# Performance work log

Hardware: AMD Instinct MI355X
Metric: run time of the kernel (lower is better)

## Reference

```python
import jax, jax.numpy as jnp
import numpy as np

L, D, F, H = 6, 512, 2048, 8
DH = D // H
SCALE = DH ** -0.5
B, S = 2, 2048


def _ln(x, w, b):
    m = jnp.mean(x, axis=-1, keepdims=True)
    v = jnp.var(x, axis=-1, keepdims=True)
    return (x - m) * jax.lax.rsqrt(v + 1e-5) * w + b


def setup_inputs() -> dict:
    key = jax.random.key(0)
    ks = jax.random.split(key, 10)
    s = 0.02
    return {
        "x": jax.random.normal(ks[0], (B, S, D), jnp.float32),
        "mask": jnp.zeros((B, 1, 1, S), jnp.float32),
        "ln1_w": jnp.ones((L, D), jnp.float32),
        "ln1_b": jnp.zeros((L, D), jnp.float32),
        "in_w": s * jax.random.normal(ks[1], (L, D, 3 * D), jnp.float32),
        "in_b": jnp.zeros((L, 3 * D), jnp.float32),
        "out_w": s * jax.random.normal(ks[2], (L, D, D), jnp.float32),
        "out_b": jnp.zeros((L, D), jnp.float32),
        "ln2_w": jnp.ones((L, D), jnp.float32),
        "ln2_b": jnp.zeros((L, D), jnp.float32),
        "ffn1_w": s * jax.random.normal(ks[3], (L, D, F), jnp.float32),
        "ffn1_b": jnp.zeros((L, F), jnp.float32),
        "ffn2_w": s * jax.random.normal(ks[4], (L, F, D), jnp.float32),
        "ffn2_b": jnp.zeros((L, D), jnp.float32),
        "norm_w": jnp.ones((D,), jnp.float32),
        "norm_b": jnp.zeros((D,), jnp.float32),
    }


def reference(x, mask, ln1_w, ln1_b, in_w, in_b, out_w, out_b,
              ln2_w, ln2_b, ffn1_w, ffn1_b, ffn2_w, ffn2_b, norm_w, norm_b):
    def step(h, p):
        (l1w, l1b, iw, ib, ow, ob, l2w, l2b, f1w, f1b, f2w, f2b) = p
        # --- self-attention (pre-norm) ---
        y = _ln(h, l1w, l1b)
        proj = y @ iw + ib                       # [B,S,3D]
        q, k, v = jnp.split(proj, 3, axis=-1)    # each [B,S,D]
        q = q.reshape(B, S, H, DH)
        k = k.reshape(B, S, H, DH)
        v = v.reshape(B, S, H, DH)
        dot = jnp.einsum('bqhd,bkhd->bhqk', q * SCALE, k) + mask  # [B,H,S,S]
        att = jax.nn.softmax(dot, axis=-1)
        o = jnp.einsum('bhqk,bkhd->bqhd', att, v).reshape(B, S, D)
        h = o @ ow + ob + h
        # --- FFN (pre-norm) ---
        y = _ln(h, l2w, l2b)
        y = jax.nn.relu(y @ f1w + f1b) @ f2w + f2b
        return h + y, None

    params = (ln1_w, ln1_b, in_w, in_b, out_w, out_b,
              ln2_w, ln2_b, ffn1_w, ffn1_b, ffn2_w, ffn2_b)
    x, _ = jax.lax.scan(step, x, params)
    return _ln(x, norm_w, norm_b)
```

## Files before the change

kernel.cpp:

```cpp
#include <hip/hip_runtime.h>
#include <hip/hip_bf16.h>
#include <stdint.h>


typedef __bf16 bf16x8 __attribute__((ext_vector_type(8)));
typedef __bf16 bf16x4 __attribute__((ext_vector_type(4)));
typedef float f32x4 __attribute__((ext_vector_type(4)));
typedef unsigned short u16;
typedef unsigned short u16x8 __attribute__((ext_vector_type(8)));

#define NB 2
#define NS 2048
#define ND 512
#define NH 8
#define NDH 64
#define NF 2048
#define NL 6
#define NCHUNK 8
#define CK (NS / NCHUNK)
#define LOG2E 1.4426950408889634f
#define QSCALE (0.125f * LOG2E)

#if defined(__has_builtin)
#if __has_builtin(__builtin_amdgcn_global_load_lds)
#define HAVE_GLDS 1
#endif
#endif
#ifndef HAVE_GLDS
#define HAVE_GLDS 0
#endif

#if HAVE_GLDS
__device__ __forceinline__ void glds16(const u16* g, u16* l) {
  __builtin_amdgcn_global_load_lds(
      (const __attribute__((address_space(1))) unsigned int*)g,
      (__attribute__((address_space(3))) unsigned int*)l, 16, 0, 0);
}
#endif

__device__ __forceinline__ u16 f2bf(float f) {
  unsigned u = __float_as_uint(f);
  u += 0x7FFFu + ((u >> 16) & 1u);
  return (u16)(u >> 16);
}

__global__ __launch_bounds__(256) void wcvt_t(const float* __restrict__ src,
                                              u16* __restrict__ dst,
                                              int K, int N) {
  __shared__ float tile[32][33];
  int l = blockIdx.z;
  const float* s = src + (size_t)l * K * N;
  u16* d = dst + (size_t)l * K * N;
  int k0 = blockIdx.y * 32, n0 = blockIdx.x * 32;
  int tx = threadIdx.x, ty = threadIdx.y;
  for (int i = 0; i < 32; i += 8)
    tile[ty + i][tx] = s[(size_t)(k0 + ty + i) * N + n0 + tx];
  __syncthreads();
  for (int i = 0; i < 32; i += 8)
    d[(size_t)(n0 + ty + i) * K + k0 + tx] = f2bf(tile[tx][ty + i]);
}

template <int OUT_BF16>
__global__ __launch_bounds__(256) void ln_k(const float* __restrict__ x,
                                            const float* __restrict__ w,
                                            const float* __restrict__ b,
                                            void* __restrict__ out) {
  int row = blockIdx.x;
  int t = threadIdx.x;
  const float* xr = x + (size_t)row * ND;
  float2 v = ((const float2*)xr)[t];
  float s = v.x + v.y, ss = v.x * v.x + v.y * v.y;
  for (int o = 32; o > 0; o >>= 1) {
    s += __shfl_down(s, o);
    ss += __shfl_down(ss, o);
  }
  __shared__ float rs[4], rss[4];
  if ((t & 63) == 0) { rs[t >> 6] = s; rss[t >> 6] = ss; }
  __syncthreads();
  float S = rs[0] + rs[1] + rs[2] + rs[3];
  float SS = rss[0] + rss[1] + rss[2] + rss[3];
  float mean = S * (1.0f / ND);
  float var = SS * (1.0f / ND) - mean * mean;
  float rstd = rsqrtf(var + 1e-5f);
  float2 wv = ((const float2*)w)[t];
  float2 bv = ((const float2*)b)[t];
  float y0 = (v.x - mean) * rstd * wv.x + bv.x;
  float y1 = (v.y - mean) * rstd * wv.y + bv.y;
  if (OUT_BF16) {
    ushort2 p; p.x = f2bf(y0); p.y = f2bf(y1);
    ((ushort2*)out)[(size_t)row * (ND / 2) + t] = p;
  } else {
    float2 p; p.x = y0; p.y = y1;
    ((float2*)out)[(size_t)row * (ND / 2) + t] = p;
  }
}

template <int EPI, int BM, int BN, int BK, int KSPLIT = 1>
__global__ __launch_bounds__(256) void gemm_bt(const u16* __restrict__ A,
                                               const u16* __restrict__ Bt,
                                               const float* __restrict__ bias,
                                               const float* __restrict__ resid,
                                               void* __restrict__ C,
                                               int M, int N, int K) {
  constexpr int MT = BM / 32;
  constexpr int NT = BN / 32;
  constexpr int CB = BK / 8;
  constexpr int RPP = 2048 / BK;
  constexpr int AP = BM / RPP;
  constexpr int BP = BN / RPP;
  constexpr int KK = BK / 32;
  __shared__ u16 la[BM * BK];
  __shared__ u16 lb[BN * BK];
  int bm = blockIdx.y, bn = blockIdx.x;
  int kc = (KSPLIT > 1) ? blockIdx.z : 0;
  int klen = K / KSPLIT;
  int kbase = kc * klen;
  int t = threadIdx.x;
  int wave = t >> 6, lane = t & 63, quad = lane >> 4, l15 = lane & 15;
  int wm = (wave >> 1) * (BM / 2), wn = (wave & 1) * (BN / 2);
  f32x4 acc[MT][NT] = {};
  int srow = t / CB;
  int scol = ((t % CB) ^ (srow & (CB - 1))) * 8;
  const u16* Ag = A + (size_t)(bm * BM) * K + kbase;
  const u16* Bg = Bt + (size_t)(bn * BN) * K + kbase;
#if HAVE_GLDS
  u16* laB = la + wave * 512;
  u16* lbB = lb + wave * 512;
#endif
  for (int k0 = 0; k0 < klen; k0 += BK) {
    __syncthreads();
#if HAVE_GLDS
#pragma unroll
    for (int g = 0; g < AP; g++)
      glds16(&Ag[(size_t)(srow + g * RPP) * K + k0 + scol], laB + g * 2048);
#pragma unroll
    for (int g = 0; g < BP; g++)
      glds16(&Bg[(size_t)(srow + g * RPP) * K + k0 + scol], lbB + g * 2048);
#else
#pragma unroll
    for (int g = 0; g < AP; g++)
      *(bf16x8*)&la[(srow + g * RPP) * BK + (t % CB) * 8] =
          *(const bf16x8*)&Ag[(size_t)(srow + g * RPP) * K + k0 + scol];
#pragma unroll
    for (int g = 0; g < BP; g++)
      *(bf16x8*)&lb[(srow + g * RPP) * BK + (t % CB) * 8] =
          *(const bf16x8*)&Bg[(size_t)(srow + g * RPP) * K + k0 + scol];
#endif
    __syncthreads();
#pragma unroll
    for (int kk = 0; kk < KK; kk++) {
      bf16x8 af[MT], bfr[NT];
#pragma unroll
      for (int i = 0; i < MT; i++) {
        int row = wm + i * 16 + l15;
        af[i] = *(const bf16x8*)&la[row * BK + ((kk * 4 + quad) ^ (row & (CB - 1))) * 8];
      }
#pragma unroll
      for (int i = 0; i < NT; i++) {
        int row = wn + i * 16 + l15;
        bfr[i] = *(const bf16x8*)&lb[row * BK + ((kk * 4 + quad) ^ (row & (CB - 1))) * 8];
      }
#pragma unroll
      for (int mt = 0; mt < MT; mt++)
#pragma unroll
        for (int nt = 0; nt < NT; nt++)
          acc[mt][nt] = __builtin_amdgcn_mfma_f32_16x16x32_bf16(
              af[mt], bfr[nt], acc[mt][nt], 0, 0, 0);
    }
  }
#pragma unroll
  for (int mt = 0; mt < MT; mt++)
#pragma unroll
    for (int nt = 0; nt < NT; nt++) {
      int col = bn * BN + wn + nt * 16 + l15;
      float bcol = (EPI == 3 || EPI == 4) ? 0.f : bias[col];
#pragma unroll
      for (int r = 0; r < 4; r++) {
        int row = bm * BM + wm + mt * 16 + quad * 4 + r;
        float v = acc[mt][nt][r] + ((EPI == 3) ? bias[row] : bcol);
        if (EPI == 1) v = fmaxf(v, 0.f);
        if (EPI == 2)
          ((float*)C)[(size_t)row * N + col] = v + resid[(size_t)row * N + col];
        else if (EPI == 4)
          ((u16*)C)[(size_t)kc * M * N + (size_t)row * N + col] = f2bf(v);
        else
          ((u16*)C)[(size_t)row * N + col] = f2bf(v);
      }
    }
}

__global__ __launch_bounds__(256) void ksplit_red(const u16* __restrict__ part,
                                                  const float* __restrict__ bias,
                                                  const float* __restrict__ resid,
                                                  float* __restrict__ out) {
  int gt = blockIdx.x * 256 + threadIdx.x;
  int col = (gt & 63) * 8;
  int row = gt >> 6;
  size_t base = (size_t)row * ND + col;
  float acc[8];
#pragma unroll
  for (int j = 0; j < 8; j++) acc[j] = bias[col + j] + resid[base + j];
#pragma unroll
  for (int c = 0; c < 4; c++) {
    bf16x8 v = *(const bf16x8*)&part[(size_t)c * (NB * NS) * ND + base];
#pragma unroll
    for (int j = 0; j < 8; j++) acc[j] += (float)v[j];
  }
#pragma unroll
  for (int j = 0; j < 2; j++)
    *(float4*)&out[base + j * 4] =
        make_float4(acc[j * 4], acc[j * 4 + 1], acc[j * 4 + 2], acc[j * 4 + 3]);
}

__global__ __launch_bounds__(256) void attn_k(const u16* __restrict__ qk,
                                              const u16* __restrict__ vt,
                                              const float* __restrict__ mask,
                                              u16* __restrict__ opart,
                                              float* __restrict__ lbuf) {
  __shared__ u16 kt_s[64 * 64];
  __shared__ u16 vt_s[64 * 64];
  __shared__ u16 p_s[4][16 * 68];
  int bh = blockIdx.y;
  int b = bh >> 3, h = bh & 7;
  int qt = blockIdx.x;
  int c = blockIdx.z;
  int t = threadIdx.x;
  int wave = t >> 6, lane = t & 63, quad = lane >> 4, l15 = lane & 15;

  int qrow = qt * 64 + wave * 16 + l15;
  const u16* qbase = qk + ((size_t)(b * NS + qrow)) * (2 * ND) + h * NDH;
  bf16x8 qf[2];
  qf[0] = *(const bf16x8*)&qbase[quad * 8];
  qf[1] = *(const bf16x8*)&qbase[32 + quad * 8];
#pragma unroll
  for (int e = 0; e < 8; e++) {
    qf[0][e] = (__bf16)((float)qf[0][e] * QSCALE);
    qf[1][e] = (__bf16)((float)qf[1][e] * QSCALE);
  }
  bf16x8 ones;
#pragma unroll
  for (int e = 0; e < 8; e++) ones[e] = (__bf16)1.0f;

  f32x4 oacc[4] = {};
  f32x4 ls = {};

  int srow8 = t >> 3;
  int segsw = ((t & 7) ^ ((t >> 3) & 7)) * 8;
  const u16* kg0 = qk + ((size_t)(b * NS + srow8)) * (2 * ND) + ND + h * NDH + segsw;
  const u16* vg0 = vt + ((size_t)(h * NDH + srow8)) * (NB * NS) + b * NS + segsw;
#if HAVE_GLDS
  u16* ktB = kt_s + wave * 512;
  u16* vtB = vt_s + wave * 512;
#endif
  for (int kt0 = c * CK; kt0 < (c + 1) * CK; kt0 += 64) {
    float m2[4];
#pragma unroll
    for (int nt = 0; nt < 4; nt++)
      m2[nt] = mask[b * NS + kt0 + nt * 16 + l15] * LOG2E;
    __syncthreads();
#if HAVE_GLDS
    glds16(&kg0[(size_t)kt0 * (2 * ND)], ktB);
    glds16(&kg0[(size_t)(kt0 + 32) * (2 * ND)], ktB + 2048);
    glds16(&vg0[kt0], vtB);
    glds16(&vg0[kt0 + (size_t)32 * (NB * NS)], vtB + 2048);
#else
    *(bf16x8*)&kt_s[srow8 * 64 + (t & 7) * 8] =
        *(const bf16x8*)&kg0[(size_t)kt0 * (2 * ND)];
    *(bf16x8*)&kt_s[(srow8 + 32) * 64 + (t & 7) * 8] =
        *(const bf16x8*)&kg0[(size_t)(kt0 + 32) * (2 * ND)];
    *(bf16x8*)&vt_s[srow8 * 64 + (t & 7) * 8] = *(const bf16x8*)&vg0[kt0];
    *(bf16x8*)&vt_s[(srow8 + 32) * 64 + (t & 7) * 8] =
        *(const bf16x8*)&vg0[kt0 + (size_t)32 * (NB * NS)];
#endif
    __syncthreads();
    f32x4 sc[4] = {};
#pragma unroll
    for (int nt = 0; nt < 4; nt++) {
      int row = nt * 16 + l15;
      bf16x8 kf0 = *(const bf16x8*)&kt_s[row * 64 + (quad ^ (row & 7)) * 8];
      bf16x8 kf1 = *(const bf16x8*)&kt_s[row * 64 + ((quad + 4) ^ (row & 7)) * 8];
      sc[nt] = __builtin_amdgcn_mfma_f32_16x16x32_bf16(qf[0], kf0, sc[nt], 0, 0, 0);
      sc[nt] = __builtin_amdgcn_mfma_f32_16x16x32_bf16(qf[1], kf1, sc[nt], 0, 0, 0);
    }
    u16* pw = &p_s[wave][0];
#pragma unroll
    for (int nt = 0; nt < 4; nt++) {
#pragma unroll
      for (int rp = 0; rp < 2; rp++) {
        float2 pp;
        pp.x = __builtin_amdgcn_exp2f(sc[nt][2 * rp] + m2[nt]);
        pp.y = __builtin_amdgcn_exp2f(sc[nt][2 * rp + 1] + m2[nt]);
        __hip_bfloat162 bb = __float22bfloat162_rn(pp);
        ushort2 us = *reinterpret_cast<ushort2*>(&bb);
        pw[(quad * 4 + 2 * rp) * 68 + nt * 16 + l15] = us.x;
        pw[(quad * 4 + 2 * rp + 1) * 68 + nt * 16 + l15] = us.y;
      }
    }
    asm volatile("s_waitcnt lgkmcnt(0)" ::: "memory");
#pragma unroll
    for (int kk = 0; kk < 2; kk++) {
      bf16x4 plo = *(const bf16x4*)&pw[l15 * 68 + kk * 32 + quad * 8];
      bf16x4 phi = *(const bf16x4*)&pw[l15 * 68 + kk * 32 + quad * 8 + 4];
      bf16x8 pf = __builtin_shufflevector(plo, phi, 0, 1, 2, 3, 4, 5, 6, 7);
#pragma unroll
      for (int nt = 0; nt < 4; nt++) {
        int row = nt * 16 + l15;
        bf16x8 vf = *(const bf16x8*)&vt_s[row * 64 + ((kk * 4 + quad) ^ (row & 7)) * 8];
        oacc[nt] = __builtin_amdgcn_mfma_f32_16x16x32_bf16(pf, vf, oacc[nt], 0, 0, 0);
      }
      ls = __builtin_amdgcn_mfma_f32_16x16x32_bf16(pf, ones, ls, 0, 0, 0);
    }
  }
  u16* ob = opart + (((size_t)(c * NB * NH + bh) * NS) + qt * 64 + wave * 16) * NDH;
#pragma unroll
  for (int nt = 0; nt < 4; nt++)
#pragma unroll
    for (int r = 0; r < 4; r++)
      ob[(size_t)(quad * 4 + r) * NDH + nt * 16 + l15] = f2bf(oacc[nt][r]);
  if (l15 == 0) {
    size_t li = (size_t)(c * NB * NH + bh) * NS + qt * 64 + wave * 16 + quad * 4;
#pragma unroll
    for (int r = 0; r < 4; r++) lbuf[li + r] = ls[r];
  }
}

__global__ __launch_bounds__(256) void attn_merge(const u16* __restrict__ opart,
                                                  const float* __restrict__ lbuf,
                                                  u16* __restrict__ o) {
  int gt = blockIdx.x * 256 + threadIdx.x;
  int grp = gt & 7;
  int s = (gt >> 3) & (NS - 1);
  int bh = gt >> 14;
  float L = 0.f;
#pragma unroll
  for (int c = 0; c < NCHUNK; c++)
    L += lbuf[(size_t)(c * NB * NH + bh) * NS + s];
  float inv = 1.0f / L;
  float acc[8] = {};
#pragma unroll
  for (int c = 0; c < NCHUNK; c++) {
    bf16x8 ov = *(const bf16x8*)&opart[((size_t)(c * NB * NH + bh) * NS + s) * NDH + grp * 8];
#pragma unroll
    for (int j = 0; j < 8; j++) acc[j] += (float)ov[j];
  }
  u16x8 res;
#pragma unroll
  for (int j = 0; j < 8; j++) res[j] = f2bf(acc[j] * inv);
  int b = bh >> 3, h = bh & 7;
  *(u16x8*)&o[((size_t)(b * NS + s)) * ND + h * NDH + grp * 8] = res;
}

extern "C" void kernel_launch(void* const* d_in, const int* in_sizes, int n_in,
                              void* d_out, int out_size, void* d_ws, size_t ws_size,
                              hipStream_t stream) {
  const float* x = (const float*)d_in[0];
  const float* mask = (const float*)d_in[1];
  const float* ln1w = (const float*)d_in[2];
  const float* ln1b = (const float*)d_in[3];
  const float* in_w = (const float*)d_in[4];
  const float* in_b = (const float*)d_in[5];
  const float* out_w = (const float*)d_in[6];
  const float* out_b = (const float*)d_in[7];
  const float* ln2w = (const float*)d_in[8];
  const float* ln2b = (const float*)d_in[9];
  const float* f1w = (const float*)d_in[10];
  const float* f1b = (const float*)d_in[11];
  const float* f2w = (const float*)d_in[12];
  const float* f2b = (const float*)d_in[13];
  const float* normw = (const float*)d_in[14];
  const float* normb = (const float*)d_in[15];

  char* ws = (char*)d_ws;
  auto carve = [&](size_t bytes) {
    char* p = ws;
    ws += (bytes + 255) & ~(size_t)255;
    return p;
  };
  u16* wq_t = (u16*)carve((size_t)NL * 3 * ND * ND * 2);
  u16* wo_t = (u16*)carve((size_t)NL * ND * ND * 2);
  u16* w1_t = (u16*)carve((size_t)NL * NF * ND * 2);
  u16* w2_t = (u16*)carve((size_t)NL * ND * NF * 2);
  u16* ybuf = (u16*)carve((size_t)NB * NS * ND * 2);
  u16* qk = (u16*)carve((size_t)NB * NS * 2 * ND * 2);
  u16* vtb = (u16*)carve((size_t)ND * NB * NS * 2);
  u16* obuf = (u16*)carve((size_t)NB * NS * ND * 2);
  u16* ubuf = (u16*)carve((size_t)NB * NS * NF * 2);
  float* hA = (float*)carve((size_t)NB * NS * ND * 4);
  float* hB = (float*)carve((size_t)NB * NS * ND * 4);
  float* lbuf = (float*)carve((size_t)NCHUNK * NB * NH * NS * 4);
  u16* opart = (u16*)carve((size_t)NCHUNK * NB * NH * NS * NDH * 2);
  u16* pbuf = (u16*)carve((size_t)4 * NB * NS * ND * 2);

  const int M = NB * NS;
  dim3 tb(32, 8);
  wcvt_t<<<dim3(3 * ND / 32, ND / 32, NL), tb, 0, stream>>>(in_w, wq_t, ND, 3 * ND);
  wcvt_t<<<dim3(ND / 32, ND / 32, NL), tb, 0, stream>>>(out_w, wo_t, ND, ND);
  wcvt_t<<<dim3(NF / 32, ND / 32, NL), tb, 0, stream>>>(f1w, w1_t, ND, NF);
  wcvt_t<<<dim3(ND / 32, NF / 32, NL), tb, 0, stream>>>(f2w, w2_t, NF, ND);

  const float* hin = x;
  for (int l = 0; l < NL; l++) {
    ln_k<1><<<M, 256, 0, stream>>>(hin, ln1w + l * ND, ln1b + l * ND, ybuf);
    gemm_bt<0, 64, 128, 128><<<dim3(2 * ND / 128, M / 64), 256, 0, stream>>>(
        ybuf, wq_t + (size_t)l * 3 * ND * ND, in_b + l * 3 * ND, nullptr, qk,
        M, 2 * ND, ND);
    gemm_bt<3, 64, 64, 128><<<dim3(M / 64, ND / 64), 256, 0, stream>>>(
        wq_t + (size_t)l * 3 * ND * ND + (size_t)2 * ND * ND, ybuf,
        in_b + l * 3 * ND + 2 * ND, nullptr, vtb, ND, M, ND);
    attn_k<<<dim3(NS / 64, NB * NH, NCHUNK), 256, 0, stream>>>(
        qk, vtb, mask, opart, lbuf);
    attn_merge<<<(NB * NH * NS * 8) / 256, 256, 0, stream>>>(opart, lbuf, obuf);
    gemm_bt<2, 64, 64, 128><<<dim3(ND / 64, M / 64), 256, 0, stream>>>(
        obuf, wo_t + (size_t)l * ND * ND, out_b + l * ND, hin, hB, M, ND, ND);
    ln_k<1><<<M, 256, 0, stream>>>(hB, ln2w + l * ND, ln2b + l * ND, ybuf);
    gemm_bt<1, 128, 128, 64><<<dim3(NF / 128, M / 128), 256, 0, stream>>>(
        ybuf, w1_t + (size_t)l * NF * ND, f1b + l * NF, nullptr, ubuf, M, NF, ND);
    gemm_bt<4, 128, 128, 64, 4><<<dim3(ND / 128, M / 128, 4), 256, 0, stream>>>(
        ubuf, w2_t + (size_t)l * ND * NF, nullptr, nullptr, pbuf, M, ND, NF);
    ksplit_red<<<(M * ND / 8) / 256, 256, 0, stream>>>(
        pbuf, f2b + l * ND, hB, hA);
    hin = hA;
  }
  ln_k<0><<<M, 256, 0, stream>>>(hA, normw, normb, (float*)d_out);
}
```

Baseline: 849.3 us.

## Fuse QKV GEMMs, fold layernorms into split-K reductions, halve attention chunks

Merges the QK and V projection GEMMs into one launch that dispatches on block id. The out-projection becomes a 4-way split-K GEMM whose reduction kernel also adds bias and residual and applies the following layernorm. The FFN2 reduction likewise applies the next layer's LN1, or the final norm on the last layer. Attention key chunks drop from 8 to 4. The goal is fewer launches and fewer full-activation round trips, at the cost of bf16 partial-sum rounding in the out-projection and less parallelism in attention.

```diff
diff --git a/kernel.cpp b/kernel.cpp
--- a/kernel.cpp
+++ b/kernel.cpp
@@ -16,7 +16,7 @@
 #define NDH 64
 #define NF 2048
 #define NL 6
-#define NCHUNK 8
+#define NCHUNK 4
 #define CK (NS / NCHUNK)
 #define LOG2E 1.4426950408889634f
 #define QSCALE (0.125f * LOG2E)
@@ -60,11 +60,10 @@
     d[(size_t)(n0 + ty + i) * K + k0 + tx] = f2bf(tile[tx][ty + i]);
 }
 
-template <int OUT_BF16>
 __global__ __launch_bounds__(256) void ln_k(const float* __restrict__ x,
                                             const float* __restrict__ w,
                                             const float* __restrict__ b,
-                                            void* __restrict__ out) {
+                                            u16* __restrict__ out) {
   int row = blockIdx.x;
   int t = threadIdx.x;
   const float* xr = x + (size_t)row * ND;
@@ -84,24 +83,21 @@
   float rstd = rsqrtf(var + 1e-5f);
   float2 wv = ((const float2*)w)[t];
   float2 bv = ((const float2*)b)[t];
-  float y0 = (v.x - mean) * rstd * wv.x + bv.x;
-  float y1 = (v.y - mean) * rstd * wv.y + bv.y;
-  if (OUT_BF16) {
-    ushort2 p; p.x = f2bf(y0); p.y = f2bf(y1);
-    ((ushort2*)out)[(size_t)row * (ND / 2) + t] = p;
-  } else {
-    float2 p; p.x = y0; p.y = y1;
-    ((float2*)out)[(size_t)row * (ND / 2) + t] = p;
-  }
-}
-
-template <int EPI, int BM, int BN, int BK, int KSPLIT = 1>
-__global__ __launch_bounds__(256) void gemm_bt(const u16* __restrict__ A,
-                                               const u16* __restrict__ Bt,
-                                               const float* __restrict__ bias,
-                                               const float* __restrict__ resid,
-                                               void* __restrict__ C,
-                                               int M, int N, int K) {
+  ushort2 p;
+  p.x = f2bf((v.x - mean) * rstd * wv.x + bv.x);
+  p.y = f2bf((v.y - mean) * rstd * wv.y + bv.y);
+  ((ushort2*)out)[(size_t)row * (ND / 2) + t] = p;
+}
+
+template <int EPI, int BM, int BN, int BK, int KSPLIT>
+__device__ __forceinline__ void gemm_dev(u16* la, u16* lb,
+                                         const u16* __restrict__ A,
+                                         const u16* __restrict__ Bt,
+                                         const float* __restrict__ bias,
+                                         const float* __restrict__ resid,
+                                         void* __restrict__ C,
+                                         int M, int N, int K,
+                                         int bm, int bn, int kc, int t) {
   constexpr int MT = BM / 32;
   constexpr int NT = BN / 32;
   constexpr int CB = BK / 8;
@@ -109,13 +105,8 @@
   constexpr int AP = BM / RPP;
   constexpr int BP = BN / RPP;
   constexpr int KK = BK / 32;
-  __shared__ u16 la[BM * BK];
-  __shared__ u16 lb[BN * BK];
-  int bm = blockIdx.y, bn = blockIdx.x;
-  int kc = (KSPLIT > 1) ? blockIdx.z : 0;
   int klen = K / KSPLIT;
   int kbase = kc * klen;
-  int t = threadIdx.x;
   int wave = t >> 6, lane = t & 63, quad = lane >> 4, l15 = lane & 15;
   int wm = (wave >> 1) * (BM / 2), wn = (wave & 1) * (BN / 2);
   f32x4 acc[MT][NT] = {};
@@ -189,13 +180,51 @@
     }
 }
 
-__global__ __launch_bounds__(256) void ksplit_red(const u16* __restrict__ part,
-                                                  const float* __restrict__ bias,
-                                                  const float* __restrict__ resid,
-                                                  float* __restrict__ out) {
-  int gt = blockIdx.x * 256 + threadIdx.x;
-  int col = (gt & 63) * 8;
-  int row = gt >> 6;
+template <int EPI, int BM, int BN, int BK, int KSPLIT = 1>
+__global__ __launch_bounds__(256) void gemm_bt(const u16* __restrict__ A,
+                                               const u16* __restrict__ Bt,
+                                               const float* __restrict__ bias,
+                                               const float* __restrict__ resid,
+                                               void* __restrict__ C,
+                                               int M, int N, int K) {
+  __shared__ u16 la[BM * BK];
+  __shared__ u16 lb[BN * BK];
+  gemm_dev<EPI, BM, BN, BK, KSPLIT>(la, lb, A, Bt, bias, resid, C, M, N, K,
+                                    blockIdx.y, blockIdx.x,
+                                    (KSPLIT > 1) ? blockIdx.z : 0, threadIdx.x);
+}
+
+__global__ __launch_bounds__(256) void qkv_fused(const u16* __restrict__ y,
+                                                 const u16* __restrict__ wqk,
+                                                 const u16* __restrict__ wv,
+                                                 const float* __restrict__ inb,
+                                                 u16* __restrict__ qkout,
+                                                 u16* __restrict__ vtout) {
+  __shared__ u16 smem[(64 + 128) * 128];
+  int id = blockIdx.x, t = threadIdx.x;
+  const int M = NB * NS;
+  if (id < 512) {
+    gemm_dev<0, 64, 128, 128, 1>(smem, smem + 64 * 128, y, wqk, inb, nullptr,
+                                 qkout, M, 2 * ND, ND, id >> 3, id & 7, 0, t);
+  } else {
+    id -= 512;
+    gemm_dev<3, 64, 64, 128, 1>(smem, smem + 64 * 128, wv, y, inb + 2 * ND,
+                                nullptr, vtout, ND, M, ND, id >> 6, id & 63, 0, t);
+  }
+}
+
+template <int OUT_BF16>
+__global__ __launch_bounds__(256) void red_ln(const u16* __restrict__ part,
+                                              const float* __restrict__ bias,
+                                              const float* __restrict__ resid,
+                                              const float* __restrict__ lw,
+                                              const float* __restrict__ lbb,
+                                              float* __restrict__ hout,
+                                              void* __restrict__ yout) {
+  int t = threadIdx.x;
+  int row = blockIdx.x * 4 + (t >> 6);
+  int lane = t & 63;
+  int col = lane * 8;
   size_t base = (size_t)row * ND + col;
   float acc[8];
 #pragma unroll
@@ -206,10 +235,34 @@
 #pragma unroll
     for (int j = 0; j < 8; j++) acc[j] += (float)v[j];
   }
-#pragma unroll
-  for (int j = 0; j < 2; j++)
-    *(float4*)&out[base + j * 4] =
-        make_float4(acc[j * 4], acc[j * 4 + 1], acc[j * 4 + 2], acc[j * 4 + 3]);
+  *(float4*)&hout[base] = make_float4(acc[0], acc[1], acc[2], acc[3]);
+  *(float4*)&hout[base + 4] = make_float4(acc[4], acc[5], acc[6], acc[7]);
+  float s = 0.f, ss = 0.f;
+#pragma unroll
+  for (int j = 0; j < 8; j++) { s += acc[j]; ss += acc[j] * acc[j]; }
+  for (int o = 1; o < 64; o <<= 1) {
+    s += __shfl_xor(s, o);
+    ss += __shfl_xor(ss, o);
+  }
+  float mean = s * (1.0f / ND);
+  float var = ss * (1.0f / ND) - mean * mean;
+  float rstd = rsqrtf(var + 1e-5f);
+  float4 w0 = *(const float4*)&lw[col], w1 = *(const float4*)&lw[col + 4];
+  float4 b0 = *(const float4*)&lbb[col], b1 = *(const float4*)&lbb[col + 4];
+  float wv[8] = {w0.x, w0.y, w0.z, w0.w, w1.x, w1.y, w1.z, w1.w};
+  float bv[8] = {b0.x, b0.y, b0.z, b0.w, b1.x, b1.y, b1.z, b1.w};
+  float yv[8];
+#pragma unroll
+  for (int j = 0; j < 8; j++) yv[j] = (acc[j] - mean) * rstd * wv[j] + bv[j];
+  if (OUT_BF16) {
+    u16x8 res;
+#pragma unroll
+    for (int j = 0; j < 8; j++) res[j] = f2bf(yv[j]);
+    *(u16x8*)&((u16*)yout)[base] = res;
+  } else {
+    *(float4*)&((float*)yout)[base] = make_float4(yv[0], yv[1], yv[2], yv[3]);
+    *(float4*)&((float*)yout)[base + 4] = make_float4(yv[4], yv[5], yv[6], yv[7]);
+  }
 }
 
 __global__ __launch_bounds__(256) void attn_k(const u16* __restrict__ qk,
@@ -398,28 +451,32 @@
   wcvt_t<<<dim3(NF / 32, ND / 32, NL), tb, 0, stream>>>(f1w, w1_t, ND, NF);
   wcvt_t<<<dim3(ND / 32, NF / 32, NL), tb, 0, stream>>>(f2w, w2_t, NF, ND);
 
+  ln_k<<<M, 256, 0, stream>>>(x, ln1w, ln1b, ybuf);
+
   const float* hin = x;
   for (int l = 0; l < NL; l++) {
-    ln_k<1><<<M, 256, 0, stream>>>(hin, ln1w + l * ND, ln1b + l * ND, ybuf);
-    gemm_bt<0, 64, 128, 128><<<dim3(2 * ND / 128, M / 64), 256, 0, stream>>>(
-        ybuf, wq_t + (size_t)l * 3 * ND * ND, in_b + l * 3 * ND, nullptr, qk,
-        M, 2 * ND, ND);
-    gemm_bt<3, 64, 64, 128><<<dim3(M / 64, ND / 64), 256, 0, stream>>>(
-        wq_t + (size_t)l * 3 * ND * ND + (size_t)2 * ND * ND, ybuf,
-        in_b + l * 3 * ND + 2 * ND, nullptr, vtb, ND, M, ND);
+    qkv_fused<<<1024, 256, 0, stream>>>(
+        ybuf, wq_t + (size_t)l * 3 * ND * ND,
+        wq_t + (size_t)l * 3 * ND * ND + (size_t)2 * ND * ND,
+        in_b + l * 3 * ND, qk, vtb);
     attn_k<<<dim3(NS / 64, NB * NH, NCHUNK), 256, 0, stream>>>(
         qk, vtb, mask, opart, lbuf);
     attn_merge<<<(NB * NH * NS * 8) / 256, 256, 0, stream>>>(opart, lbuf, obuf);
-    gemm_bt<2, 64, 64, 128><<<dim3(ND / 64, M / 64), 256, 0, stream>>>(
-        obuf, wo_t + (size_t)l * ND * ND, out_b + l * ND, hin, hB, M, ND, ND);
-    ln_k<1><<<M, 256, 0, stream>>>(hB, ln2w + l * ND, ln2b + l * ND, ybuf);
+    gemm_bt<4, 128, 128, 64, 4><<<dim3(ND / 128, M / 128, 4), 256, 0, stream>>>(
+        obuf, wo_t + (size_t)l * ND * ND, nullptr, nullptr, pbuf, M, ND, ND);
+    red_ln<1><<<M / 4, 256, 0, stream>>>(pbuf, out_b + l * ND, hin,
+                                         ln2w + l * ND, ln2b + l * ND, hB, ybuf);
     gemm_bt<1, 128, 128, 64><<<dim3(NF / 128, M / 128), 256, 0, stream>>>(
         ybuf, w1_t + (size_t)l * NF * ND, f1b + l * NF, nullptr, ubuf, M, NF, ND);
     gemm_bt<4, 128, 128, 64, 4><<<dim3(ND / 128, M / 128, 4), 256, 0, stream>>>(
         ubuf, w2_t + (size_t)l * ND * NF, nullptr, nullptr, pbuf, M, ND, NF);
-    ksplit_red<<<(M * ND / 8) / 256, 256, 0, stream>>>(
-        pbuf, f2b + l * ND, hB, hA);
+    if (l < NL - 1)
+      red_ln<1><<<M / 4, 256, 0, stream>>>(pbuf, f2b + l * ND, hB,
+                                           ln1w + (l + 1) * ND,
+                                           ln1b + (l + 1) * ND, hA, ybuf);
+    else
+      red_ln<0><<<M / 4, 256, 0, stream>>>(pbuf, f2b + l * ND, hB,
+                                           normw, normb, hA, (float*)d_out);
     hin = hA;
   }
-  ln_k<0><<<M, 256, 0, stream>>>(hA, normw, normb, (float*)d_out);
-}
+}
```

Result: no change. 838.1 us (-1.3%).
